# Kernel optimization log

Measured on AMD Instinct MI355X. Metric: run time of the kernel, lower is better.

## Reference

```python
import jax, jax.numpy as jnp
import numpy as np

B, T, C = 4, 1024, 1024
H, HKV, N = 16, 8, 64
REP = H // HKV
D_LORA, D_MV, D_GATE = 64, 32, 160
EPS = 1e-06
ROPE_THETA = 1000000.0


def setup_inputs() -> dict:
    key = jax.random.key(0)
    ks = jax.random.split(key, 20)
    def s(i, shape, sc=0.02, off=0.0):
        return jax.random.normal(ks[i], shape, jnp.float32) * sc + off
    return {
        "x": jax.random.normal(ks[0], (B, T, C), jnp.float32),
        "v_first": jax.random.normal(ks[1], (B, T, C), jnp.float32),
        "Wr": s(2, (C, H * N)), "Wk": s(3, (C, HKV * N)), "Wv": s(4, (C, HKV * N)), "Wo": s(5, (H * N, C)),
        "w0": s(6, (C,), 0.1, -4.0), "w1": s(7, (C, D_LORA)), "w2": s(8, (D_LORA, C)),
        "a0": s(9, (C,), 0.1), "a1": s(10, (C, D_LORA)), "a2": s(11, (D_LORA, C)),
        "v0": s(12, (C,), 0.1, 0.73), "v1": s(13, (C, D_MV)), "v2": s(14, (D_MV, C)),
        "g1": s(15, (C, D_GATE)), "g2": s(16, (D_GATE, C)),
        "r_k": s(17, (H, N), 0.1, -0.04),
        "r_norm_w": jnp.ones((N,), jnp.float32), "k_norm_w": jnp.ones((N,), jnp.float32),
    }


def rms_norm(x, w):
    var = jnp.mean(jnp.square(x.astype(jnp.float32)), axis=-1, keepdims=True)
    return w * (x.astype(jnp.float32) * jax.lax.rsqrt(var + EPS))


def rope_cos_sin(t, n):
    half = n // 2
    inv_freq = 1.0 / ROPE_THETA ** (jnp.arange(half, dtype=jnp.float32) / half)
    freqs = jnp.arange(t, dtype=jnp.float32)[:, None] * inv_freq[None, :]
    emb = jnp.concatenate([freqs, freqs], axis=-1)  # [T, N]
    # broadcast to [1, T, 1, N] (unsqueeze_dim=2 in the original)
    return jnp.cos(emb)[None, :, None, :], jnp.sin(emb)[None, :, None, :]


def rotate_half(x):
    x1, x2 = jnp.split(x, 2, axis=-1)
    return jnp.concatenate([-x2, x1], axis=-1)


def wkv7(r, dec, k, v, a, b):
    # RWKV-7 state recurrence. All inputs [B,T,H,N]; state S: [B,H,N_v,N_k].
    # S_t = S_{t-1} * diag(dec_t) + (S_{t-1} @ a_t) b_t^T + v_t k_t^T ; y_t = S_t r_t
    def step(S, ins):
        rt, wt, kt, vt, at, bt = ins  # each [B,H,N]
        S = S * wt[:, :, None, :] \
            + jnp.einsum('bhij,bhj,bhk->bhik', S, at, bt) \
            + vt[..., None] * kt[..., None, :]
        return S, jnp.einsum('bhij,bhj->bhi', S, rt)
    ins = tuple(jnp.moveaxis(t, 1, 0) for t in (r, dec, k, v, a, b))  # [T,B,H,N]
    S0 = jnp.zeros((r.shape[0], H, N, N), r.dtype)
    _, ys = jax.lax.scan(step, S0, ins)
    return jnp.moveaxis(ys, 0, 1)  # [B,T,H,N]


def _forward(x, v_first, Wr, Wk, Wv, Wo, w0, w1, w2, a0, a1, a2, v0, v1, v2, g1, g2, r_k, r_norm_w, k_norm_w):
    Bq, Tq = x.shape[0], x.shape[1]
    r = rms_norm((x @ Wr).reshape(Bq, Tq, H, N), r_norm_w)
    k = rms_norm((x @ Wk).reshape(Bq, Tq, HKV, N), k_norm_w)
    # w = -softplus(-(w0 + tanh(x@w1)@w2)) - 0.5 ; kernel decay = exp(-exp(w))
    w = -jax.nn.softplus(-(w0 + jnp.tanh(x @ w1) @ w2)) - 0.5  # [B,T,C]
    v = (x @ Wv).reshape(Bq, Tq, HKV, N)
    cos, sin = rope_cos_sin(Tq, N)
    r = r * cos + rotate_half(r) * sin
    k = k * cos + rotate_half(k) * sin
    k = jnp.repeat(k, REP, axis=2)  # GQA repeat -> [B,T,H,N]
    v = jnp.repeat(v, REP, axis=2)
    # layer_id != 0: residual value mixing with first-layer value
    mix = jax.nn.sigmoid(v0 + (x @ v1) @ v2).reshape(Bq, Tq, H, N)
    v = v + (v_first.reshape(Bq, Tq, H, N) - v) * mix
    a = jax.nn.sigmoid(a0 + (x @ a1) @ a2).reshape(Bq, Tq, H, N)
    g = jax.nn.sigmoid(x @ g1) @ g2  # [B,T,C]
    kk = k / jnp.maximum(jnp.linalg.norm(k, axis=-1, keepdims=True), 1e-12)  # F.normalize per head
    dec = jnp.exp(-jnp.exp(w)).reshape(Bq, Tq, H, N)
    y = wkv7(r, dec, k, v, -kk, kk * a)  # [B,T,H,N]
    y = y + jnp.sum(r * k * r_k, axis=-1, keepdims=True) * v
    out = (y.reshape(Bq, Tq, H * N) * g) @ Wo
    return out


def reference(x, v_first, Wr, Wk, Wv, Wo, w0, w1, w2, a0, a1, a2, v0, v1, v2, g1, g2, r_k, r_norm_w, k_norm_w):
    out = _forward(x, v_first, Wr, Wk, Wv, Wo, w0, w1, w2, a0, a1, a2, v0, v1, v2, g1, g2, r_k, r_norm_w, k_norm_w)
    return (out, v_first)
```

## Files before the change

kernel.cpp:

```cpp
#include <hip/hip_runtime.h>
#include <math.h>
#include <stdint.h>

#define Bb   4
#define Tt   1024
#define Cc   1024
#define Hh   16
#define HKVn 8
#define Nn   64
#define MT   (Bb*Tt)
#define NC   32
#define CL   32
#define NCAT 2432

typedef __bf16 bf16x8_t __attribute__((ext_vector_type(8)));
typedef float  f32x4_t  __attribute__((ext_vector_type(4)));

__device__ __forceinline__ uint16_t f2bf(float f) {
    uint32_t u = __float_as_uint(f);
    uint32_t r = (u + 0x7fffu + ((u >> 16) & 1u)) >> 16;
    return (uint16_t)r;
}

__device__ __forceinline__ float rlane(float v, int l) {
    return __uint_as_float(__builtin_amdgcn_readlane(__float_as_uint(v), l));
}

__device__ __forceinline__ void stage64(const float* g, float* l, int lane) {
    __builtin_amdgcn_global_load_lds(
        (const __attribute__((address_space(1))) uint32_t*)(g + lane),
        (__attribute__((address_space(3))) uint32_t*)l, 4, 0, 0);
}

__global__ __launch_bounds__(256) void transpose_all_kernel(
    const float* __restrict__ Wr, const float* __restrict__ Wk, const float* __restrict__ Wv,
    const float* __restrict__ w1, const float* __restrict__ a1, const float* __restrict__ v1,
    const float* __restrict__ g1, const float* __restrict__ Wo,
    const float* __restrict__ w2, const float* __restrict__ a2,
    const float* __restrict__ v2, const float* __restrict__ g2,
    uint16_t* __restrict__ WCAT, uint16_t* __restrict__ WoT,
    uint16_t* __restrict__ LW, uint16_t* __restrict__ LA,
    uint16_t* __restrict__ LV, uint16_t* __restrict__ LG,
    const float* __restrict__ x, uint16_t* __restrict__ xb,
    const float4* __restrict__ vfi, float4* __restrict__ out2)
{
    int z = blockIdx.z;
    if (z == 12) {
        int bid = blockIdx.y * 32 + blockIdx.x;
        int tid0 = bid * 256 + threadIdx.x;
        #pragma unroll
        for (int it = 0; it < 4; ++it) {
            int i = tid0 + it * (1024 * 256);
            float4 v = reinterpret_cast<const float4*>(x)[i];
            ushort4 o;
            o.x = f2bf(v.x); o.y = f2bf(v.y); o.z = f2bf(v.z); o.w = f2bf(v.w);
            reinterpret_cast<ushort4*>(xb)[i] = o;
            out2[i] = vfi[i];
        }
        return;
    }
    const float* W; int Nsrc, Ndst, Ksrc, Kout, off; uint16_t* out;
    switch (z) {
        case 0:  W = Wr; Nsrc = 1024; Ndst = 1024; Ksrc = 1024; Kout = 1024; off = 0;    out = WCAT; break;
        case 1:  W = Wk; Nsrc = 512;  Ndst = 512;  Ksrc = 1024; Kout = 1024; off = 1024; out = WCAT; break;
        case 2:  W = Wv; Nsrc = 512;  Ndst = 512;  Ksrc = 1024; Kout = 1024; off = 1536; out = WCAT; break;
        case 3:  W = w1; Nsrc = 64;   Ndst = 64;   Ksrc = 1024; Kout = 1024; off = 2048; out = WCAT; break;
        case 4:  W = a1; Nsrc = 64;   Ndst = 64;   Ksrc = 1024; Kout = 1024; off = 2112; out = WCAT; break;
        case 5:  W = v1; Nsrc = 32;   Ndst = 64;   Ksrc = 1024; Kout = 1024; off = 2176; out = WCAT; break;
        case 6:  W = g1; Nsrc = 160;  Ndst = 192;  Ksrc = 1024; Kout = 1024; off = 2240; out = WCAT; break;
        case 7:  W = Wo; Nsrc = 1024; Ndst = 1024; Ksrc = 1024; Kout = 1024; off = 0;    out = WoT;  break;
        case 8:  W = w2; Nsrc = 1024; Ndst = 1024; Ksrc = 64;   Kout = 64;   off = 0;    out = LW;   break;
        case 9:  W = a2; Nsrc = 1024; Ndst = 1024; Ksrc = 64;   Kout = 64;   off = 0;    out = LA;   break;
        case 10: W = v2; Nsrc = 1024; Ndst = 1024; Ksrc = 32;   Kout = 64;   off = 0;    out = LV;   break;
        default: W = g2; Nsrc = 1024; Ndst = 1024; Ksrc = 160;  Kout = 192;  off = 0;    out = LG;   break;
    }
    int n0 = blockIdx.x * 32, k0 = blockIdx.y * 32;
    if (n0 >= Ndst || k0 >= Kout) return;
    __shared__ float tile[32][33];
    int tx = threadIdx.x & 31, ty = threadIdx.x >> 5;
    #pragma unroll
    for (int i = 0; i < 32; i += 8) {
        int k = k0 + ty + i, n = n0 + tx;
        tile[ty + i][tx] = (k < Ksrc && n < Nsrc) ? W[(size_t)k * Nsrc + n] : 0.f;
    }
    __syncthreads();
    #pragma unroll
    for (int i = 0; i < 32; i += 8) {
        int n = n0 + ty + i, k = k0 + tx;
        if (n < Ndst) out[(size_t)(off + n) * Kout + k] = f2bf(tile[tx][ty + i]);
    }
}

__global__ __launch_bounds__(256) void gemm_bf16_proj(
    const uint16_t* __restrict__ A, const uint16_t* __restrict__ Bt,
    int M, int N, int K,
    float* __restrict__ R_, float* __restrict__ K_, float* __restrict__ V_,
    uint16_t* __restrict__ W1b, uint16_t* __restrict__ A1b,
    uint16_t* __restrict__ V1b, uint16_t* __restrict__ G1b)
{
    __shared__ __align__(16) uint16_t As[128 * 64];
    __shared__ __align__(16) uint16_t Bs[128 * 64];
    int tid  = threadIdx.x;
    int lane = tid & 63, wid = tid >> 6;
    int wm = (wid >> 1) * 64, wn = (wid & 1) * 64;
    int bm = blockIdx.y * 128, bn = blockIdx.x * 128;

    f32x4_t acc[4][4];
    #pragma unroll
    for (int i = 0; i < 4; ++i)
        #pragma unroll
        for (int j = 0; j < 4; ++j)
            #pragma unroll
            for (int e = 0; e < 4; ++e) acc[i][j][e] = 0.f;

    int rowS[4], kbS[4];
    #pragma unroll
    for (int i = 0; i < 4; ++i) {
        int d = (i * 256 + tid) * 16;
        int row = d >> 7;
        int kb = (d & 127) ^ ((row & 7) << 4);
        rowS[i] = row; kbS[i] = kb >> 1;
    }

    for (int k0 = 0; k0 < K; k0 += 64) {
        #pragma unroll
        for (int i = 0; i < 4; ++i) {
            const uint16_t* srcA = A + (size_t)(bm + rowS[i]) * K + k0 + kbS[i];
            uint16_t* ldsA = As + (i * 256 + wid * 64) * 8;
            __builtin_amdgcn_global_load_lds(
                (const __attribute__((address_space(1))) uint32_t*)srcA,
                (__attribute__((address_space(3))) uint32_t*)ldsA, 16, 0, 0);
            int nr = bn + rowS[i];
            const uint16_t* srcB = Bt + (size_t)(nr < N ? nr : 0) * K + k0 + kbS[i];
            uint16_t* ldsB = Bs + (i * 256 + wid * 64) * 8;
            __builtin_amdgcn_global_load_lds(
                (const __attribute__((address_space(1))) uint32_t*)srcB,
                (__attribute__((address_space(3))) uint32_t*)ldsB, 16, 0, 0);
        }
        __syncthreads();

        #pragma unroll
        for (int kk = 0; kk < 64; kk += 32) {
            int fb = (kk + ((lane >> 4) << 3)) << 1;
            bf16x8_t af[4], bfr[4];
            #pragma unroll
            for (int i = 0; i < 4; ++i) {
                int row = wm + i * 16 + (lane & 15);
                int byteA = (row << 7) + (fb ^ ((row & 7) << 4));
                af[i] = *reinterpret_cast<const bf16x8_t*>(
                    reinterpret_cast<const char*>(As) + byteA);
                int col = wn + i * 16 + (lane & 15);
                int byteB = (col << 7) + (fb ^ ((col & 7) << 4));
                bfr[i] = *reinterpret_cast<const bf16x8_t*>(
                    reinterpret_cast<const char*>(Bs) + byteB);
            }
            #pragma unroll
            for (int i = 0; i < 4; ++i)
                #pragma unroll
                for (int j = 0; j < 4; ++j)
                    acc[i][j] = __builtin_amdgcn_mfma_f32_16x16x32_bf16(
                        af[i], bfr[j], acc[i][j], 0, 0, 0);
        }
        __syncthreads();
    }

    #pragma unroll
    for (int i = 0; i < 4; ++i) {
        int row0 = bm + wm + i * 16 + ((lane >> 4) << 2);
        #pragma unroll
        for (int j = 0; j < 4; ++j) {
            int col = bn + wn + j * 16 + (lane & 15);
            if (col >= N) continue;
            #pragma unroll
            for (int rg = 0; rg < 4; ++rg) {
                float v = acc[i][j][rg];
                int row = row0 + rg;
                if (col < 1024)       R_[(size_t)row * 1024 + col] = v;
                else if (col < 1536)  K_[(size_t)row * 512 + (col - 1024)] = v;
                else if (col < 2048)  V_[(size_t)row * 512 + (col - 1536)] = v;
                else if (col < 2112)  W1b[(size_t)row * 64 + (col - 2048)] = f2bf(tanhf(v));
                else if (col < 2176)  A1b[(size_t)row * 64 + (col - 2112)] = f2bf(v);
                else if (col < 2240)  V1b[(size_t)row * 64 + (col - 2176)] = f2bf(v);
                else                  G1b[(size_t)row * 192 + (col - 2240)] = f2bf(1.f / (1.f + expf(-v)));
            }
        }
    }
}

__global__ __launch_bounds__(256) void gemm_bf16(
    const uint16_t* __restrict__ A, const uint16_t* __restrict__ Bt,
    float* __restrict__ C, int M, int N, int K)
{
    __shared__ __align__(16) uint16_t As[128 * 64];
    __shared__ __align__(16) uint16_t Bs[128 * 64];
    int tid  = threadIdx.x;
    int lane = tid & 63, wid = tid >> 6;
    int wm = (wid >> 1) * 64, wn = (wid & 1) * 64;
    int bm = blockIdx.y * 128, bn = blockIdx.x * 128;

    f32x4_t acc[4][4];
    #pragma unroll
    for (int i = 0; i < 4; ++i)
        #pragma unroll
        for (int j = 0; j < 4; ++j)
            #pragma unroll
            for (int e = 0; e < 4; ++e) acc[i][j][e] = 0.f;

    int rowS[4], kbS[4];
    #pragma unroll
    for (int i = 0; i < 4; ++i) {
        int d = (i * 256 + tid) * 16;
        int row = d >> 7;
        int kb = (d & 127) ^ ((row & 7) << 4);
        rowS[i] = row; kbS[i] = kb >> 1;
    }

    for (int k0 = 0; k0 < K; k0 += 64) {
        #pragma unroll
        for (int i = 0; i < 4; ++i) {
            const uint16_t* srcA = A + (size_t)(bm + rowS[i]) * K + k0 + kbS[i];
            uint16_t* ldsA = As + (i * 256 + wid * 64) * 8;
            __builtin_amdgcn_global_load_lds(
                (const __attribute__((address_space(1))) uint32_t*)srcA,
                (__attribute__((address_space(3))) uint32_t*)ldsA, 16, 0, 0);
            int nr = bn + rowS[i];
            const uint16_t* srcB = Bt + (size_t)(nr < N ? nr : 0) * K + k0 + kbS[i];
            uint16_t* ldsB = Bs + (i * 256 + wid * 64) * 8;
            __builtin_amdgcn_global_load_lds(
                (const __attribute__((address_space(1))) uint32_t*)srcB,
                (__attribute__((address_space(3))) uint32_t*)ldsB, 16, 0, 0);
        }
        __syncthreads();

        #pragma unroll
        for (int kk = 0; kk < 64; kk += 32) {
            int fb = (kk + ((lane >> 4) << 3)) << 1;
            bf16x8_t af[4], bfr[4];
            #pragma unroll
            for (int i = 0; i < 4; ++i) {
                int row = wm + i * 16 + (lane & 15);
                int byteA = (row << 7) + (fb ^ ((row & 7) << 4));
                af[i] = *reinterpret_cast<const bf16x8_t*>(
                    reinterpret_cast<const char*>(As) + byteA);
                int col = wn + i * 16 + (lane & 15);
                int byteB = (col << 7) + (fb ^ ((col & 7) << 4));
                bfr[i] = *reinterpret_cast<const bf16x8_t*>(
                    reinterpret_cast<const char*>(Bs) + byteB);
            }
            #pragma unroll
            for (int i = 0; i < 4; ++i)
                #pragma unroll
                for (int j = 0; j < 4; ++j)
                    acc[i][j] = __builtin_amdgcn_mfma_f32_16x16x32_bf16(
                        af[i], bfr[j], acc[i][j], 0, 0, 0);
        }
        __syncthreads();
    }

    #pragma unroll
    for (int i = 0; i < 4; ++i) {
        int row0 = bm + wm + i * 16 + ((lane >> 4) << 2);
        #pragma unroll
        for (int j = 0; j < 4; ++j) {
            int col = bn + wn + j * 16 + (lane & 15);
            if (col >= N) continue;
            #pragma unroll
            for (int rg = 0; rg < 4; ++rg)
                C[(size_t)(row0 + rg) * N + col] = acc[i][j][rg];
        }
    }
}

__global__ __launch_bounds__(256) void lora2_mfma(
    const uint16_t* __restrict__ W1b, const uint16_t* __restrict__ A1b,
    const uint16_t* __restrict__ V1b, const uint16_t* __restrict__ G1b,
    const uint16_t* __restrict__ LW, const uint16_t* __restrict__ LA,
    const uint16_t* __restrict__ LV, const uint16_t* __restrict__ LG,
    const float* __restrict__ w0, const float* __restrict__ a0, const float* __restrict__ v0,
    const float* __restrict__ VRAW, const float* __restrict__ vfi,
    const float* __restrict__ ABUF,
    float* __restrict__ DEC, float* __restrict__ AARR,
    float* __restrict__ VFIN, float* __restrict__ GARR)
{
    int seg = blockIdx.x & 3;
    int bn = (blockIdx.x >> 2) * 128;
    int bm = blockIdx.y * 128;

    const uint16_t* A; const uint16_t* Bt; int K;
    if (seg == 0)      { A = W1b; Bt = LW; K = 64; }
    else if (seg == 1) { A = A1b; Bt = LA; K = 64; }
    else if (seg == 2) { A = V1b; Bt = LV; K = 64; }
    else               { A = G1b; Bt = LG; K = 192; }

    __shared__ __align__(16) uint16_t As[128 * 64];
    __shared__ __align__(16) uint16_t Bs[128 * 64];
    int tid  = threadIdx.x;
    int lane = tid & 63, wid = tid >> 6;
    int wm = (wid >> 1) * 64, wn = (wid & 1) * 64;

    f32x4_t acc[4][4];
    #pragma unroll
    for (int i = 0; i < 4; ++i)
        #pragma unroll
        for (int j = 0; j < 4; ++j)
            #pragma unroll
            for (int e = 0; e < 4; ++e) acc[i][j][e] = 0.f;

    int rowS[4], kbS[4];
    #pragma unroll
    for (int i = 0; i < 4; ++i) {
        int d = (i * 256 + tid) * 16;
        int row = d >> 7;
        int kb = (d & 127) ^ ((row & 7) << 4);
        rowS[i] = row; kbS[i] = kb >> 1;
    }

    for (int k0 = 0; k0 < K; k0 += 64) {
        #pragma unroll
        for (int i = 0; i < 4; ++i) {
            const uint16_t* srcA = A + (size_t)(bm + rowS[i]) * K + k0 + kbS[i];
            uint16_t* ldsA = As + (i * 256 + wid * 64) * 8;
            __builtin_amdgcn_global_load_lds(
                (const __attribute__((address_space(1))) uint32_t*)srcA,
                (__attribute__((address_space(3))) uint32_t*)ldsA, 16, 0, 0);
            const uint16_t* srcB = Bt + (size_t)(bn + rowS[i]) * K + k0 + kbS[i];
            uint16_t* ldsB = Bs + (i * 256 + wid * 64) * 8;
            __builtin_amdgcn_global_load_lds(
                (const __attribute__((address_space(1))) uint32_t*)srcB,
                (__attribute__((address_space(3))) uint32_t*)ldsB, 16, 0, 0);
        }
        __syncthreads();

        #pragma unroll
        for (int kk = 0; kk < 64; kk += 32) {
            int fb = (kk + ((lane >> 4) << 3)) << 1;
            bf16x8_t af[4], bfr[4];
            #pragma unroll
            for (int i = 0; i < 4; ++i) {
                int row = wm + i * 16 + (lane & 15);
                int byteA = (row << 7) + (fb ^ ((row & 7) << 4));
                af[i] = *reinterpret_cast<const bf16x8_t*>(
                    reinterpret_cast<const char*>(As) + byteA);
                int col = wn + i * 16 + (lane & 15);
                int byteB = (col << 7) + (fb ^ ((col & 7) << 4));
                bfr[i] = *reinterpret_cast<const bf16x8_t*>(
                    reinterpret_cast<const char*>(Bs) + byteB);
            }
            #pragma unroll
            for (int i = 0; i < 4; ++i)
                #pragma unroll
                for (int j = 0; j < 4; ++j)
                    acc[i][j] = __builtin_amdgcn_mfma_f32_16x16x32_bf16(
                        af[i], bfr[j], acc[i][j], 0, 0, 0);
        }
        __syncthreads();
    }

    #pragma unroll
    for (int i = 0; i < 4; ++i) {
        int row0 = bm + wm + i * 16 + ((lane >> 4) << 2);
        #pragma unroll
        for (int j = 0; j < 4; ++j) {
            int col = bn + wn + j * 16 + (lane & 15);
            #pragma unroll
            for (int rg = 0; rg < 4; ++rg) {
                float v = acc[i][j][rg];
                int row = row0 + rg;
                if (seg == 0) {
                    float z = v + w0[col];
                    float sig = 1.f / (1.f + expf(-z));
                    DEC[(size_t)row * 1024 + col] = expf(-0.6065306597f * sig);
                } else if (seg == 1) {
                    float kk = -ABUF[(size_t)row * 512 + ((col >> 7) << 6) + (col & 63)];
                    AARR[(size_t)row * 1024 + col] = kk / (1.f + expf(-(v + a0[col])));
                } else if (seg == 2) {
                    float m = 1.f / (1.f + expf(-(v + v0[col])));
                    float vr = VRAW[(size_t)row * 512 + ((col >> 7) << 6) + (col & 63)];
                    float vf = vfi[(size_t)row * 1024 + col];
                    VFIN[(size_t)row * 1024 + col] = vr + (vf - vr) * m;
                } else {
                    GARR[(size_t)row * 1024 + col] = v;
                }
            }
        }
    }
}

__global__ __launch_bounds__(256) void normrope_prep(
    float* __restrict__ RRAW, float* __restrict__ KRAW,
    float* __restrict__ ABUF,
    const float* __restrict__ rnw, const float* __restrict__ knw,
    const float* __restrict__ rk,
    float* __restrict__ BON)
{
    int unit = blockIdx.x * 4 + (threadIdx.x >> 6);
    int hk = unit & 7;
    int bt = unit >> 3;
    int b = bt >> 10, t = bt & 1023;
    int lane = threadIdx.x & 63;
    int fi = lane & 31;
    float invf = powf(1.0e6f, -(float)fi * (1.0f / 32.0f));
    float fr = (float)t * invf;
    float c = cosf(fr), s = sinf(fr);

    size_t kidx = ((size_t)bt * 8 + hk) * 64 + lane;
    float k = KRAW[kidx];
    float ss = k * k;
    #pragma unroll
    for (int m = 1; m < 64; m <<= 1) ss += __shfl_xor(ss, m, 64);
    float kn = k * rsqrtf(ss * (1.f / 64.f) + 1e-6f) * knw[lane];
    float kp = __shfl_xor(kn, 32, 64);
    float kroped = fmaf(kn, c, ((lane < 32) ? -kp : kp) * s);
    KRAW[kidx] = kroped;

    float ss2 = kroped * kroped;
    #pragma unroll
    for (int m = 1; m < 64; m <<= 1) ss2 += __shfl_xor(ss2, m, 64);
    float kk = kroped / fmaxf(sqrtf(ss2), 1e-12f);
    ABUF[kidx] = -kk;

    #pragma unroll
    for (int rep = 0; rep < 2; ++rep) {
        int h = hk * 2 + rep;
        size_t cidx = (size_t)bt * 1024 + h * 64 + lane;
        float r = RRAW[cidx];
        float ssr = r * r;
        #pragma unroll
        for (int m = 1; m < 64; m <<= 1) ssr += __shfl_xor(ssr, m, 64);
        float rn = r * rsqrtf(ssr * (1.f / 64.f) + 1e-6f) * rnw[lane];
        float rp = __shfl_xor(rn, 32, 64);
        float rroped = fmaf(rn, c, ((lane < 32) ? -rp : rp) * s);
        RRAW[cidx] = rroped;

        float bon = rroped * kroped * rk[h * 64 + lane];
        #pragma unroll
        for (int m = 1; m < 64; m <<= 1) bon += __shfl_xor(bon, m, 64);
        if (lane == 0) BON[((size_t)(b * 16 + h)) * 1024 + t] = bon;
    }
}

__global__ __launch_bounds__(64) void wkv_pass1(
    const float* __restrict__ R, const float* __restrict__ Kv,
    const float* __restrict__ Ab, const float* __restrict__ Bhat,
    const float* __restrict__ Dd, const float* __restrict__ Vv,
    float* __restrict__ Q, float* __restrict__ Y0,
    float* __restrict__ PLT, float* __restrict__ ZL)
{
    int blk = blockIdx.x;
    int c   = blk & (NC - 1);
    int bh  = blk >> 5;
    int h   = bh & 15;
    int b   = bh >> 4;
    int hk  = h >> 1;
    int lane = threadIdx.x;
    int t0 = c * CL;

    size_t cb = ((size_t)(b * 1024 + t0)) * 1024 + h * 64;
    size_t kb = ((size_t)(b * 1024 + t0)) * 512 + hk * 64;
    size_t qb = (((size_t)bh) * 1024 + t0) * 64;

    __shared__ __align__(16) float sA[2][64], sB[2][64], sD[2][64],
                                   sR[2][64], sK[2][64], sV[2][64];

    float SP[64], SZ[64];
    #pragma unroll
    for (int j = 0; j < 64; ++j) { SP[j] = (j == lane) ? 1.f : 0.f; SZ[j] = 0.f; }

    auto stage = [&](int u, int buf) {
        stage64(Ab   + kb + (size_t)u * 512,  &sA[buf][0], lane);
        stage64(Bhat + cb + (size_t)u * 1024, &sB[buf][0], lane);
        stage64(Dd   + cb + (size_t)u * 1024, &sD[buf][0], lane);
        stage64(R    + cb + (size_t)u * 1024, &sR[buf][0], lane);
        stage64(Kv   + kb + (size_t)u * 512,  &sK[buf][0], lane);
        stage64(Vv   + cb + (size_t)u * 1024, &sV[buf][0], lane);
    };
    stage(0, 0);

    for (int u = 0; u < CL; ++u) {
        int un = (u + 1 < CL) ? u + 1 : u;
        stage(un, (u + 1) & 1);
        asm volatile("s_waitcnt vmcnt(6)" ::: "memory");
        int cur = u & 1;
        float v = sV[cur][lane];

        float pa0 = 0.f, pa1 = 0.f, za0 = 0.f, za1 = 0.f;
        #pragma unroll
        for (int jc = 0; jc < 16; ++jc) {
            float4 a4 = *reinterpret_cast<const float4*>(&sA[cur][jc * 4]);
            pa0 = fmaf(SP[jc*4+0], a4.x, pa0); za0 = fmaf(SZ[jc*4+0], a4.x, za0);
            pa1 = fmaf(SP[jc*4+1], a4.y, pa1); za1 = fmaf(SZ[jc*4+1], a4.y, za1);
            pa0 = fmaf(SP[jc*4+2], a4.z, pa0); za0 = fmaf(SZ[jc*4+2], a4.z, za0);
            pa1 = fmaf(SP[jc*4+3], a4.w, pa1); za1 = fmaf(SZ[jc*4+3], a4.w, za1);
        }
        float pa = pa0 + pa1;
        float za = za0 + za1;

        float q0 = 0.f, q1 = 0.f, y0a = 0.f, y1a = 0.f;
        #pragma unroll
        for (int jc = 0; jc < 16; ++jc) {
            float4 d4 = *reinterpret_cast<const float4*>(&sD[cur][jc * 4]);
            float4 b4 = *reinterpret_cast<const float4*>(&sB[cur][jc * 4]);
            float4 k4 = *reinterpret_cast<const float4*>(&sK[cur][jc * 4]);
            float4 r4 = *reinterpret_cast<const float4*>(&sR[cur][jc * 4]);
            SP[jc*4+0] = fmaf(SP[jc*4+0], d4.x, pa * b4.x); q0  = fmaf(SP[jc*4+0], r4.x, q0);
            SZ[jc*4+0] = fmaf(SZ[jc*4+0], d4.x, fmaf(za, b4.x, v * k4.x)); y0a = fmaf(SZ[jc*4+0], r4.x, y0a);
            SP[jc*4+1] = fmaf(SP[jc*4+1], d4.y, pa * b4.y); q1  = fmaf(SP[jc*4+1], r4.y, q1);
            SZ[jc*4+1] = fmaf(SZ[jc*4+1], d4.y, fmaf(za, b4.y, v * k4.y)); y1a = fmaf(SZ[jc*4+1], r4.y, y1a);
            SP[jc*4+2] = fmaf(SP[jc*4+2], d4.z, pa * b4.z); q0  = fmaf(SP[jc*4+2], r4.z, q0);
            SZ[jc*4+2] = fmaf(SZ[jc*4+2], d4.z, fmaf(za, b4.z, v * k4.z)); y0a = fmaf(SZ[jc*4+2], r4.z, y0a);
            SP[jc*4+3] = fmaf(SP[jc*4+3], d4.w, pa * b4.w); q1  = fmaf(SP[jc*4+3], r4.w, q1);
            SZ[jc*4+3] = fmaf(SZ[jc*4+3], d4.w, fmaf(za, b4.w, v * k4.w)); y1a = fmaf(SZ[jc*4+3], r4.w, y1a);
        }
        Q[qb + (size_t)u * 64 + lane]    = q0 + q1;
        Y0[cb + (size_t)u * 1024 + lane] = y0a + y1a;
    }

    size_t pbT = (size_t)blk * 4096;
    #pragma unroll
    for (int j = 0; j < 64; ++j)
        PLT[pbT + j * 64 + (lane ^ ((j & 7) << 2))] = SP[j];
    size_t pb = pbT + (size_t)lane * 64;
    #pragma unroll
    for (int j = 0; j < 64; j += 4)
        *reinterpret_cast<float4*>(&ZL[pb + j]) =
            make_float4(SZ[j], SZ[j + 1], SZ[j + 2], SZ[j + 3]);
}

__global__ __launch_bounds__(256) void wkv_pass2(
    const float* __restrict__ PLT, float* ZLio)
{
    int blk = blockIdx.x;
    int rg  = blk & 3;
    int bh  = blk >> 2;
    int tid = threadIdx.x, lane = tid & 63, wv = tid >> 6;

    __shared__ __align__(16) float Pld[2][4096];
    __shared__ __align__(16) float Zld[2][1024];

    float S0 = 0.f, S1 = 0.f, S2 = 0.f, S3 = 0.f;

    auto stage = [&](int cc, int buf) {
        size_t pbase = ((size_t)bh * NC + cc) * 4096;
        #pragma unroll
        for (int i = 0; i < 4; ++i) {
            const float* src = PLT + pbase + (size_t)(i * 256 + tid) * 4;
            float* dst = &Pld[buf][(i * 256 + wv * 64) * 4];
            __builtin_amdgcn_global_load_lds(
                (const __attribute__((address_space(1))) uint32_t*)src,
                (__attribute__((address_space(3))) uint32_t*)dst, 16, 0, 0);
        }
        const float* zsrc = ZLio + pbase + (size_t)rg * 1024 + (size_t)tid * 4;
        float* zdst = &Zld[buf][wv * 256];
        __builtin_amdgcn_global_load_lds(
            (const __attribute__((address_space(1))) uint32_t*)zsrc,
            (__attribute__((address_space(3))) uint32_t*)zdst, 16, 0, 0);
    };

    stage(0, 0);

    for (int cc = 0; cc < NC; ++cc) {
        int cur = cc & 1;
        if (cc + 1 < NC) {
            stage(cc + 1, cur ^ 1);
            asm volatile("s_waitcnt vmcnt(5)" ::: "memory");
        } else {
            asm volatile("s_waitcnt vmcnt(0)" ::: "memory");
        }
        __syncthreads();

        size_t sb = ((size_t)bh * NC + cc) * 4096 + (size_t)(rg * 16 + wv * 4) * 64 + lane;
        ZLio[sb]       = S0;
        ZLio[sb + 64]  = S1;
        ZLio[sb + 128] = S2;
        ZLio[sb + 192] = S3;
        if (cc == NC - 1) break;

        int zb = (wv * 4) * 64 + lane;
        float acc0 = Zld[cur][zb],       acc1 = Zld[cur][zb + 64],
              acc2 = Zld[cur][zb + 128], acc3 = Zld[cur][zb + 192];
        const float* pcol = &Pld[cur][lane * 64];
        int swz = (lane & 7) << 2;
        #pragma unroll
        for (int m4 = 0; m4 < 64; m4 += 4) {
            float4 p4 = *reinterpret_cast<const float4*>(&pcol[m4 ^ swz]);
            #pragma unroll
            for (int s = 0; s < 4; ++s) {
                float pv = (&p4.x)[s];
                acc0 = fmaf(rlane(S0, m4 + s), pv, acc0);
                acc1 = fmaf(rlane(S1, m4 + s), pv, acc1);
                acc2 = fmaf(rlane(S2, m4 + s), pv, acc2);
                acc3 = fmaf(rlane(S3, m4 + s), pv, acc3);
            }
        }
        S0 = acc0; S1 = acc1; S2 = acc2; S3 = acc3;
        __syncthreads();
    }
}

__global__ __launch_bounds__(64) void wkv_pass3(
    const float* __restrict__ SST, const float* __restrict__ Q,
    const float* __restrict__ Vv, const float* __restrict__ G,
    const float* __restrict__ BON, const float* __restrict__ Y0,
    uint16_t* __restrict__ Yb)
{
    int blk = blockIdx.x;
    int c2 = blk & (2 * NC - 1), bh = blk >> 6, h = bh & 15, b = bh >> 4;
    int cchunk = c2 >> 1;
    int lane = threadIdx.x;
    int t0 = c2 * (CL / 2);

    __shared__ __align__(16) float qs[2][64];
    __shared__ float bons[CL / 2];
    if (lane < CL / 2) bons[lane] = BON[((size_t)bh) * 1024 + t0 + lane];

    float S[64];
    size_t sb = ((size_t)(bh * NC + cchunk)) * 4096 + (size_t)lane * 64;
    #pragma unroll
    for (int jc = 0; jc < 16; ++jc) {
        float4 s4 = *reinterpret_cast<const float4*>(&SST[sb + jc * 4]);
        S[jc*4+0] = s4.x; S[jc*4+1] = s4.y; S[jc*4+2] = s4.z; S[jc*4+3] = s4.w;
    }

    size_t cb = ((size_t)(b * 1024 + t0)) * 1024 + h * 64 + lane;
    size_t qbase = (((size_t)bh) * 1024 + t0) * 64;

    stage64(Q + qbase, &qs[0][0], lane);
    for (int u = 0; u < CL / 2; ++u) {
        int un = (u + 1 < CL / 2) ? u + 1 : u;
        stage64(Q + qbase + (size_t)un * 64, &qs[(u + 1) & 1][0], lane);
        asm volatile("s_waitcnt vmcnt(1)" ::: "memory");
        int cur = u & 1;

        float d0 = 0.f, d1 = 0.f, d2 = 0.f, d3 = 0.f;
        #pragma unroll
        for (int jc = 0; jc < 16; ++jc) {
            float4 q4 = *reinterpret_cast<const float4*>(&qs[cur][jc * 4]);
            d0 = fmaf(S[jc*4+0], q4.x, d0);
            d1 = fmaf(S[jc*4+1], q4.y, d1);
            d2 = fmaf(S[jc*4+2], q4.z, d2);
            d3 = fmaf(S[jc*4+3], q4.w, d3);
        }
        float dot = (d0 + d1) + (d2 + d3);
        float y0 = Y0[cb + (size_t)u * 1024];
        float vc = Vv[cb + (size_t)u * 1024];
        float gc = G[cb + (size_t)u * 1024];
        float bon = bons[u];
        Yb[cb + (size_t)u * 1024] = f2bf((y0 + dot + bon * vc) * gc);
    }
}

extern "C" void kernel_launch(void* const* d_in, const int* in_sizes, int n_in,
                              void* d_out, int out_size, void* d_ws, size_t ws_size,
                              hipStream_t stream)
{
    const float* x   = (const float*)d_in[0];
    const float* vfi = (const float*)d_in[1];
    const float* Wr  = (const float*)d_in[2];
    const float* Wk  = (const float*)d_in[3];
    const float* Wv  = (const float*)d_in[4];
    const float* Wo  = (const float*)d_in[5];
    const float* w0  = (const float*)d_in[6];
    const float* w1  = (const float*)d_in[7];
    const float* w2  = (const float*)d_in[8];
    const float* a0  = (const float*)d_in[9];
    const float* a1  = (const float*)d_in[10];
    const float* a2  = (const float*)d_in[11];
    const float* v0  = (const float*)d_in[12];
    const float* v1  = (const float*)d_in[13];
    const float* v2  = (const float*)d_in[14];
    const float* g1  = (const float*)d_in[15];
    const float* g2  = (const float*)d_in[16];
    const float* rk  = (const float*)d_in[17];
    const float* rnw = (const float*)d_in[18];
    const float* knw = (const float*)d_in[19];

    float* ws = (float*)d_ws;
    size_t o = 0;
    float* RRAW = ws + o; o += (size_t)MT * 1024;
    float* KRAW = ws + o; o += (size_t)MT * 512;
    float* VRAW = ws + o; o += (size_t)MT * 512;
    float* DEC  = ws + o; o += (size_t)MT * 1024;
    float* AARR = ws + o; o += (size_t)MT * 1024;
    float* GARR = ws + o; o += (size_t)MT * 1024;
    float* VFIN = ws + o; o += (size_t)MT * 1024;
    float* YARR = ws + o; o += (size_t)MT * 1024;
    float* ABUF = ws + o; o += (size_t)MT * 512;
    float* QBUF = ws + o; o += (size_t)MT * 1024;
    float* PLB  = ws + o; o += (size_t)(Bb * Hh * NC) * 4096;
    float* ZLB  = ws + o; o += (size_t)(Bb * Hh * NC) * 4096;
    float* BON  = ws + o; o += (size_t)64 * 1024;
    uint16_t* XB   = (uint16_t*)(ws + o); o += (size_t)MT * 512;
    uint16_t* WCAT = (uint16_t*)(ws + o); o += (size_t)NCAT * 512;
    uint16_t* WoT  = (uint16_t*)(ws + o); o += (size_t)1024 * 512;
    uint16_t* W1b  = (uint16_t*)(ws + o); o += (size_t)MT * 32;
    uint16_t* A1b  = (uint16_t*)(ws + o); o += (size_t)MT * 32;
    uint16_t* V1b  = (uint16_t*)(ws + o); o += (size_t)MT * 32;
    uint16_t* G1b  = (uint16_t*)(ws + o); o += (size_t)MT * 96;
    uint16_t* LW   = (uint16_t*)(ws + o); o += (size_t)1024 * 32;
    uint16_t* LA   = (uint16_t*)(ws + o); o += (size_t)1024 * 32;
    uint16_t* LV   = (uint16_t*)(ws + o); o += (size_t)1024 * 32;
    uint16_t* LG   = (uint16_t*)(ws + o); o += (size_t)1024 * 96;
    uint16_t* YB = XB;

    transpose_all_kernel<<<dim3(32, 32, 13), dim3(256), 0, stream>>>(
        Wr, Wk, Wv, w1, a1, v1, g1, Wo, w2, a2, v2, g2, WCAT, WoT, LW, LA, LV, LG,
        x, XB, (const float4*)vfi, (float4*)((float*)d_out + (size_t)MT * 1024));

    dim3 blk(256);

    gemm_bf16_proj<<<dim3(NCAT / 128, MT / 128), blk, 0, stream>>>(
        XB, WCAT, MT, NCAT, 1024, RRAW, KRAW, VRAW, W1b, A1b, V1b, G1b);

    normrope_prep<<<dim3(MT * HKVn / 4), dim3(256), 0, stream>>>(
        RRAW, KRAW, ABUF, rnw, knw, rk, BON);

    lora2_mfma<<<dim3(32, MT / 128), blk, 0, stream>>>(
        W1b, A1b, V1b, G1b, LW, LA, LV, LG, w0, a0, v0, VRAW, vfi, ABUF,
        DEC, AARR, VFIN, GARR);

    wkv_pass1<<<dim3(Bb * Hh * NC), dim3(64), 0, stream>>>(
        RRAW, KRAW, ABUF, AARR, DEC, VFIN, QBUF, YARR, PLB, ZLB);
    wkv_pass2<<<dim3(Bb * Hh * 4), dim3(256), 0, stream>>>(PLB, ZLB);
    wkv_pass3<<<dim3(Bb * Hh * NC * 2), dim3(64), 0, stream>>>(
        ZLB, QBUF, VFIN, GARR, BON, YARR, YB);

    gemm_bf16<<<dim3(1024 / 128, MT / 128), blk, 0, stream>>>(
        YB, WoT, (float*)d_out, MT, 1024, 1024);
}
```

Baseline: 395.3 us.

## Fuse RMSNorm, RoPE and k-normalize into projection GEMM epilogue

The per-head RMS norm, rotary embedding and L2 normalization of k are moved into the epilogue of the projection GEMM. Each 64-column warp tile maps to one head, so the reductions use 16-lane shuffles over registers. This removes a separate pass that read and rewrote the R and K buffers. The bonus dot product stays in a small new kernel, and the GEMM epilogue gains transcendental work and register pressure.

```diff
diff --git a/kernel.cpp b/kernel.cpp
--- a/kernel.cpp
+++ b/kernel.cpp
@@ -96,7 +96,9 @@
     int M, int N, int K,
     float* __restrict__ R_, float* __restrict__ K_, float* __restrict__ V_,
     uint16_t* __restrict__ W1b, uint16_t* __restrict__ A1b,
-    uint16_t* __restrict__ V1b, uint16_t* __restrict__ G1b)
+    uint16_t* __restrict__ V1b, uint16_t* __restrict__ G1b,
+    float* __restrict__ ABUF,
+    const float* __restrict__ rnw, const float* __restrict__ knw)
 {
     __shared__ __align__(16) uint16_t As[128 * 64];
     __shared__ __align__(16) uint16_t Bs[128 * 64];
@@ -164,27 +166,89 @@
         __syncthreads();
     }
 
-    #pragma unroll
-    for (int i = 0; i < 4; ++i) {
-        int row0 = bm + wm + i * 16 + ((lane >> 4) << 2);
-        #pragma unroll
-        for (int j = 0; j < 4; ++j) {
-            int col = bn + wn + j * 16 + (lane & 15);
-            if (col >= N) continue;
+    int col0 = bn + wn;
+    int l15 = lane & 15;
+
+    if (col0 < 1536) {
+        const float* nw = (col0 < 1024) ? rnw : knw;
+        float wgt0 = nw[l15], wgt1 = nw[l15 + 16], wgt2 = nw[l15 + 32], wgt3 = nw[l15 + 48];
+        float invf0 = powf(1.0e6f, -(float)l15 * (1.0f / 32.0f));
+        float invf1 = invf0 * 1.0e-3f;
+
+        #pragma unroll
+        for (int i = 0; i < 4; ++i) {
             #pragma unroll
             for (int rg = 0; rg < 4; ++rg) {
-                float v = acc[i][j][rg];
-                int row = row0 + rg;
-                if (col < 1024)       R_[(size_t)row * 1024 + col] = v;
-                else if (col < 1536)  K_[(size_t)row * 512 + (col - 1024)] = v;
-                else if (col < 2048)  V_[(size_t)row * 512 + (col - 1536)] = v;
-                else if (col < 2112)  W1b[(size_t)row * 64 + (col - 2048)] = f2bf(tanhf(v));
-                else if (col < 2176)  A1b[(size_t)row * 64 + (col - 2112)] = f2bf(v);
-                else if (col < 2240)  V1b[(size_t)row * 64 + (col - 2176)] = f2bf(v);
-                else                  G1b[(size_t)row * 192 + (col - 2240)] = f2bf(1.f / (1.f + expf(-v)));
+                int row = bm + wm + i * 16 + ((lane >> 4) << 2) + rg;
+                float v0 = acc[i][0][rg], v1 = acc[i][1][rg],
+                      v2 = acc[i][2][rg], v3 = acc[i][3][rg];
+                float ss = v0 * v0 + v1 * v1 + v2 * v2 + v3 * v3;
+                ss += __shfl_xor(ss, 1, 64); ss += __shfl_xor(ss, 2, 64);
+                ss += __shfl_xor(ss, 4, 64); ss += __shfl_xor(ss, 8, 64);
+                float inv = rsqrtf(ss * (1.f / 64.f) + 1e-6f);
+                float n0 = v0 * inv * wgt0, n1 = v1 * inv * wgt1,
+                      n2 = v2 * inv * wgt2, n3 = v3 * inv * wgt3;
+                float t = (float)(row & 1023);
+                float f0 = t * invf0, f1 = t * invf1;
+                float c0 = cosf(f0), s0 = sinf(f0), c1 = cosf(f1), s1 = sinf(f1);
+                float o0 = fmaf(n0, c0, -n2 * s0);
+                float o1 = fmaf(n1, c1, -n3 * s1);
+                float o2 = fmaf(n2, c0,  n0 * s0);
+                float o3 = fmaf(n3, c1,  n1 * s1);
+                if (col0 < 1024) {
+                    float* dst = R_ + (size_t)row * 1024 + col0;
+                    dst[l15] = o0; dst[l15 + 16] = o1; dst[l15 + 32] = o2; dst[l15 + 48] = o3;
+                } else {
+                    float ss2 = o0 * o0 + o1 * o1 + o2 * o2 + o3 * o3;
+                    ss2 += __shfl_xor(ss2, 1, 64); ss2 += __shfl_xor(ss2, 2, 64);
+                    ss2 += __shfl_xor(ss2, 4, 64); ss2 += __shfl_xor(ss2, 8, 64);
+                    float inv2 = 1.f / fmaxf(sqrtf(ss2), 1e-12f);
+                    int ck = col0 - 1024;
+                    float* dk = K_   + (size_t)row * 512 + ck;
+                    float* da = ABUF + (size_t)row * 512 + ck;
+                    dk[l15] = o0;        dk[l15 + 16] = o1;
+                    dk[l15 + 32] = o2;   dk[l15 + 48] = o3;
+                    da[l15] = -o0 * inv2;      da[l15 + 16] = -o1 * inv2;
+                    da[l15 + 32] = -o2 * inv2; da[l15 + 48] = -o3 * inv2;
+                }
             }
         }
-    }
+    } else {
+        #pragma unroll
+        for (int i = 0; i < 4; ++i) {
+            int row0 = bm + wm + i * 16 + ((lane >> 4) << 2);
+            #pragma unroll
+            for (int j = 0; j < 4; ++j) {
+                int col = bn + wn + j * 16 + (lane & 15);
+                #pragma unroll
+                for (int rg = 0; rg < 4; ++rg) {
+                    float v = acc[i][j][rg];
+                    int row = row0 + rg;
+                    if (col < 2048)       V_[(size_t)row * 512 + (col - 1536)] = v;
+                    else if (col < 2112)  W1b[(size_t)row * 64 + (col - 2048)] = f2bf(tanhf(v));
+                    else if (col < 2176)  A1b[(size_t)row * 64 + (col - 2112)] = f2bf(v);
+                    else if (col < 2240)  V1b[(size_t)row * 64 + (col - 2176)] = f2bf(v);
+                    else                  G1b[(size_t)row * 192 + (col - 2240)] = f2bf(1.f / (1.f + expf(-v)));
+                }
+            }
+        }
+    }
+}
+
+__global__ __launch_bounds__(256) void bon_kernel(
+    const float* __restrict__ RRAW, const float* __restrict__ KRAW,
+    const float* __restrict__ rk, float* __restrict__ BON)
+{
+    int unit = blockIdx.x * 4 + (threadIdx.x >> 6);
+    int h = unit & 15, bt = unit >> 4;
+    int b = bt >> 10, t = bt & 1023;
+    int lane = threadIdx.x & 63;
+    float r = RRAW[(size_t)bt * 1024 + h * 64 + lane];
+    float k = KRAW[(size_t)bt * 512 + (h >> 1) * 64 + lane];
+    float bon = r * k * rk[h * 64 + lane];
+    #pragma unroll
+    for (int m = 1; m < 64; m <<= 1) bon += __shfl_xor(bon, m, 64);
+    if (lane == 0) BON[((size_t)(b * 16 + h)) * 1024 + t] = bon;
 }
 
 __global__ __launch_bounds__(256) void gemm_bf16(
@@ -383,59 +447,6 @@
                 }
             }
         }
-    }
-}
-
-__global__ __launch_bounds__(256) void normrope_prep(
-    float* __restrict__ RRAW, float* __restrict__ KRAW,
-    float* __restrict__ ABUF,
-    const float* __restrict__ rnw, const float* __restrict__ knw,
-    const float* __restrict__ rk,
-    float* __restrict__ BON)
-{
-    int unit = blockIdx.x * 4 + (threadIdx.x >> 6);
-    int hk = unit & 7;
-    int bt = unit >> 3;
-    int b = bt >> 10, t = bt & 1023;
-    int lane = threadIdx.x & 63;
-    int fi = lane & 31;
-    float invf = powf(1.0e6f, -(float)fi * (1.0f / 32.0f));
-    float fr = (float)t * invf;
-    float c = cosf(fr), s = sinf(fr);
-
-    size_t kidx = ((size_t)bt * 8 + hk) * 64 + lane;
-    float k = KRAW[kidx];
-    float ss = k * k;
-    #pragma unroll
-    for (int m = 1; m < 64; m <<= 1) ss += __shfl_xor(ss, m, 64);
-    float kn = k * rsqrtf(ss * (1.f / 64.f) + 1e-6f) * knw[lane];
-    float kp = __shfl_xor(kn, 32, 64);
-    float kroped = fmaf(kn, c, ((lane < 32) ? -kp : kp) * s);
-    KRAW[kidx] = kroped;
-
-    float ss2 = kroped * kroped;
-    #pragma unroll
-    for (int m = 1; m < 64; m <<= 1) ss2 += __shfl_xor(ss2, m, 64);
-    float kk = kroped / fmaxf(sqrtf(ss2), 1e-12f);
-    ABUF[kidx] = -kk;
-
-    #pragma unroll
-    for (int rep = 0; rep < 2; ++rep) {
-        int h = hk * 2 + rep;
-        size_t cidx = (size_t)bt * 1024 + h * 64 + lane;
-        float r = RRAW[cidx];
-        float ssr = r * r;
-        #pragma unroll
-        for (int m = 1; m < 64; m <<= 1) ssr += __shfl_xor(ssr, m, 64);
-        float rn = r * rsqrtf(ssr * (1.f / 64.f) + 1e-6f) * rnw[lane];
-        float rp = __shfl_xor(rn, 32, 64);
-        float rroped = fmaf(rn, c, ((lane < 32) ? -rp : rp) * s);
-        RRAW[cidx] = rroped;
-
-        float bon = rroped * kroped * rk[h * 64 + lane];
-        #pragma unroll
-        for (int m = 1; m < 64; m <<= 1) bon += __shfl_xor(bon, m, 64);
-        if (lane == 0) BON[((size_t)(b * 16 + h)) * 1024 + t] = bon;
     }
 }
 
@@ -709,10 +720,10 @@
     dim3 blk(256);
 
     gemm_bf16_proj<<<dim3(NCAT / 128, MT / 128), blk, 0, stream>>>(
-        XB, WCAT, MT, NCAT, 1024, RRAW, KRAW, VRAW, W1b, A1b, V1b, G1b);
-
-    normrope_prep<<<dim3(MT * HKVn / 4), dim3(256), 0, stream>>>(
-        RRAW, KRAW, ABUF, rnw, knw, rk, BON);
+        XB, WCAT, MT, NCAT, 1024, RRAW, KRAW, VRAW, W1b, A1b, V1b, G1b,
+        ABUF, rnw, knw);
+
+    bon_kernel<<<dim3(MT * Hh / 4), dim3(256), 0, stream>>>(RRAW, KRAW, rk, BON);
 
     lora2_mfma<<<dim3(32, MT / 128), blk, 0, stream>>>(
         W1b, A1b, V1b, G1b, LW, LA, LV, LG, w0, a0, v0, VRAW, vfi, ABUF,
```

After: 491.9 us. +24.4%, slower.
